# Kernel tuning notes

Measured on AMD Instinct MI355X. Metric: run time of the kernel, lower is better.

Reference implementation:

```python
import jax, jax.numpy as jnp
import numpy as np
from jax import lax

FEAT_STRIDE = 16
PRE_NMS_TOP_N = 6000   # cfg['TEST'].RPN_PRE_NMS_TOP_N
POST_NMS_TOP_N = 300   # cfg['TEST'].RPN_POST_NMS_TOP_N
NMS_THRESH = 0.7       # cfg['TEST'].RPN_NMS_THRESH
MIN_SIZE = 16.0        # cfg['TEST'].RPN_MIN_SIZE
B, A, H, W = 32, 9, 128, 128
NEG_INF = jnp.float32(-1e30)


def _whctrs(a):
    w = a[2] - a[0] + 1.0
    h = a[3] - a[1] + 1.0
    return w, h, a[0] + 0.5 * (w - 1), a[1] + 0.5 * (h - 1)

def _mkanchors(ws, hs, xc, yc):
    ws = ws[:, None]; hs = hs[:, None]
    return np.hstack((xc - 0.5 * (ws - 1), yc - 0.5 * (hs - 1),
                      xc + 0.5 * (ws - 1), yc + 0.5 * (hs - 1)))

def _ratio_enum(anchor, ratios):
    w, h, xc, yc = _whctrs(anchor)
    size = w * h
    ws = np.round(np.sqrt(size / ratios))
    hs = np.round(ws * ratios)
    return _mkanchors(ws, hs, xc, yc)

def _scale_enum(anchor, scales):
    w, h, xc, yc = _whctrs(anchor)
    return _mkanchors(w * scales, h * scales, xc, yc)

def generate_anchors(base_size=16, ratios=np.array([0.5, 1.0, 2.0]), scales=np.array([8.0, 16.0, 32.0])):
    base = np.array([1, 1, base_size, base_size], dtype=np.float64) - 1
    ra = _ratio_enum(base, ratios)
    return np.vstack([_scale_enum(ra[i], scales) for i in range(ra.shape[0])]).astype(np.float32)

_BASE_ANCHORS = generate_anchors()  # (A, 4)

def _all_anchors(h, w):
    sx = np.arange(w) * FEAT_STRIDE
    sy = np.arange(h) * FEAT_STRIDE
    sx, sy = np.meshgrid(sx, sy)  # row-major (h, w) matches permute(0,2,3,1) ordering
    shifts = np.stack([sx.ravel(), sy.ravel(), sx.ravel(), sy.ravel()], axis=1).astype(np.float32)
    return jnp.asarray((shifts[:, None, :] + _BASE_ANCHORS[None, :, :]).reshape(-1, 4))  # (h*w*A, 4)

# ---- bbox_transform_inv / clip_boxes ----

def _decode(anchors, deltas):
    ws = anchors[:, 2] - anchors[:, 0] + 1.0
    hs = anchors[:, 3] - anchors[:, 1] + 1.0
    cx = anchors[:, 0] + 0.5 * ws
    cy = anchors[:, 1] + 0.5 * hs
    dx, dy, dw, dh = deltas[:, 0], deltas[:, 1], deltas[:, 2], deltas[:, 3]
    pcx = dx * ws + cx
    pcy = dy * hs + cy
    pw = jnp.exp(dw) * ws
    ph = jnp.exp(dh) * hs
    return jnp.stack([pcx - 0.5 * pw, pcy - 0.5 * ph, pcx + 0.5 * pw, pcy + 0.5 * ph], axis=1)

def _clip(b, imh, imw):
    x1 = jnp.clip(b[:, 0], 0.0, imw - 1.0)
    y1 = jnp.clip(b[:, 1], 0.0, imh - 1.0)
    x2 = jnp.clip(b[:, 2], 0.0, imw - 1.0)
    y2 = jnp.clip(b[:, 3], 0.0, imh - 1.0)
    return jnp.stack([x1, y1, x2, y2], axis=1)

# ---- greedy NMS: pick top-score box, suppress IoU > thresh, repeat POST times ----

def _nms_select(boxes, scores):
    # boxes: (PRE, 4) score-sorted; scores: (PRE,)
    areas = (boxes[:, 2] - boxes[:, 0] + 1.0) * (boxes[:, 3] - boxes[:, 1] + 1.0)

    def body(i, st):
        s, keep, valid = st
        j = jnp.argmax(s)
        keep = keep.at[i].set(j)
        valid = valid.at[i].set(s[j] > NEG_INF)
        b = boxes[j]
        xx1 = jnp.maximum(b[0], boxes[:, 0])
        yy1 = jnp.maximum(b[1], boxes[:, 1])
        xx2 = jnp.minimum(b[2], boxes[:, 2])
        yy2 = jnp.minimum(b[3], boxes[:, 3])
        inter = jnp.maximum(xx2 - xx1 + 1.0, 0.0) * jnp.maximum(yy2 - yy1 + 1.0, 0.0)
        iou = inter / jnp.maximum(areas[j] + areas - inter, 1e-6)
        s = jnp.where(iou > NMS_THRESH, NEG_INF, s)  # suppresses j itself (IoU = 1)
        return s, keep, valid

    init = (scores, jnp.zeros((POST_NMS_TOP_N,), jnp.int32), jnp.zeros((POST_NMS_TOP_N,), bool))
    _, keep, valid = lax.fori_loop(0, POST_NMS_TOP_N, body, init)
    return keep, valid

def _per_image(sc, dl, info, anchors):
    prop = _clip(_decode(anchors, dl), info[0], info[1])  # (K*A, 4)
    ws = prop[:, 2] - prop[:, 0] + 1.0
    hs = prop[:, 3] - prop[:, 1] + 1.0
    min_sz = MIN_SIZE * info[2]
    sc = jnp.where((ws >= min_sz) & (hs >= min_sz), sc, NEG_INF)
    top_s, top_i = lax.top_k(sc, PRE_NMS_TOP_N)
    cand = prop[top_i]  # (PRE, 4)
    keep, valid = _nms_select(cand, top_s)
    return cand[keep] * valid[:, None].astype(cand.dtype)  # zero-pad invalid rows

def _forward(rpn_cls_prob, rpn_bbox_pred, im_info):
    b, _, h, w = rpn_cls_prob.shape
    anchors = _all_anchors(h, w)
    scores = rpn_cls_prob[:, A:, :, :].transpose(0, 2, 3, 1).reshape(b, -1)  # (b, h*w*A)
    deltas = rpn_bbox_pred.transpose(0, 2, 3, 1).reshape(b, -1, 4)           # (b, h*w*A, 4)
    boxes = jax.vmap(lambda s, d, i: _per_image(s, d, i, anchors))(scores, deltas, im_info)
    ids = jnp.broadcast_to(jnp.arange(b, dtype=boxes.dtype)[:, None, None], (b, POST_NMS_TOP_N, 1))
    return jnp.concatenate([ids, boxes], axis=2)  # (b, POST, 5): [batch_idx, x1, y1, x2, y2]

def setup_inputs() -> dict:
    key = jax.random.key(0)
    k1, k2 = jax.random.split(key)
    rpn_cls_prob = jax.random.uniform(k1, (B, 2 * A, H, W), dtype=jnp.float32)
    rpn_bbox_pred = jax.random.normal(k2, (B, 4 * A, H, W), dtype=jnp.float32) * 0.2
    im_info = jnp.tile(jnp.array([[H * FEAT_STRIDE, W * FEAT_STRIDE, 1.0]], dtype=jnp.float32), (B, 1))
    return {"rpn_cls_prob": rpn_cls_prob, "rpn_bbox_pred": rpn_bbox_pred, "im_info": im_info}

def reference(rpn_cls_prob, rpn_bbox_pred, im_info):
    return _forward(rpn_cls_prob, rpn_bbox_pred, im_info)
```

## Files before the change

kernel.cpp:

```cpp
#include <hip/hip_runtime.h>
#include <cstdint>
#include <cstddef>

#pragma clang fp contract(off)

typedef unsigned long long u64;

#define NB 32
#define NA 9
#define NH 128
#define NW 128
#define HW (NH*NW)
#define NANCH (NA*HW)
#define PRE_N 6000
#define POST_N 300
#define CAND_CAP 8192
#define NMS_T 0.7f
#define GX_GATHER 24
#define NBOX 6144
#define CH 512

__constant__ float c_wa[9] = {184.f,368.f,736.f,128.f,256.f,512.f,88.f,176.f,352.f};
__constant__ float c_ha[9] = {96.f,192.f,384.f,128.f,256.f,512.f,176.f,352.f,704.f};

__device__ __forceinline__ float4 decode_clip(int a, int h, int w,
    float dx, float dy, float dlw, float dlh, float imh, float imw) {
  float wa = c_wa[a], ha = c_ha[a];
  float cx = (float)w * 16.0f + 8.0f;
  float cy = (float)h * 16.0f + 8.0f;
  float pcx = dx * wa + cx;
  float pcy = dy * ha + cy;
  float pw = expf(dlw) * wa;
  float ph = expf(dlh) * ha;
  float x1 = pcx - 0.5f * pw;
  float y1 = pcy - 0.5f * ph;
  float x2 = pcx + 0.5f * pw;
  float y2 = pcy + 0.5f * ph;
  float4 r;
  r.x = fminf(fmaxf(x1, 0.0f), imw - 1.0f);
  r.y = fminf(fmaxf(y1, 0.0f), imh - 1.0f);
  r.z = fminf(fmaxf(x2, 0.0f), imw - 1.0f);
  r.w = fminf(fmaxf(y2, 0.0f), imh - 1.0f);
  return r;
}

__device__ __forceinline__ unsigned score_key(float sc, float bw, float bh, float msz) {
  unsigned bits = __float_as_uint(sc);
  unsigned key = (bits & 0x80000000u) ? ~bits : (bits | 0x80000000u);
  if (!(bw >= msz && bh >= msz)) key = 0u;
  return key;
}

__device__ __forceinline__ bool sup_test4(float4 v, float ar, float4 p, float pa) {
  float xx1 = fmaxf(p.x, v.x), yy1 = fmaxf(p.y, v.y);
  float xx2 = fminf(p.z, v.z), yy2 = fminf(p.w, v.w);
  float iw = fmaxf(xx2 - xx1 + 1.0f, 0.0f);
  float ih = fmaxf(yy2 - yy1 + 1.0f, 0.0f);
  float inter = iw * ih;
  float iou = inter / fmaxf(pa + ar - inter, 1e-6f);
  return iou > NMS_T;
}

__device__ __forceinline__ u64 shfl_xor_u64(u64 x, int m) {
  int lo = __shfl_xor((int)(unsigned)x, m, 64);
  int hi = __shfl_xor((int)(unsigned)(x >> 32), m, 64);
  return ((u64)(unsigned)hi << 32) | (unsigned)lo;
}

__device__ __forceinline__ void reg_step(u64 v[8], int t, int k, int j) {
  #pragma unroll
  for (int r = 0; r < 8; ++r) {
    if ((r & j) == 0) {
      int e = (t << 3) + r;
      bool up = ((e & k) == 0);
      u64 x = v[r], y = v[r | j];
      u64 mx = x > y ? x : y, mn = x > y ? y : x;
      v[r]     = up ? mx : mn;
      v[r | j] = up ? mn : mx;
    }
  }
}

__device__ __forceinline__ void shfl_step(u64 v[8], int t, int k, int j) {
  int m = j >> 3;
  bool lower = ((t & m) == 0);
  #pragma unroll
  for (int r = 0; r < 8; ++r) {
    int e = (t << 3) + r;
    bool up = ((e & k) == 0);
    u64 pv = shfl_xor_u64(v[r], m);
    bool keepmax = (up == lower);
    u64 x = v[r];
    u64 mx = x > pv ? x : pv, mn = x > pv ? pv : x;
    v[r] = keepmax ? mx : mn;
  }
}

__device__ __forceinline__ void lds_step(u64* sm, u64 v[8], int t, int k, int j) {
  int m = j >> 3;
  __syncthreads();
  #pragma unroll
  for (int r = 0; r < 8; ++r) sm[(r << 10) | t] = v[r];
  __syncthreads();
  bool lower = ((t & m) == 0);
  bool up = (((t << 3) & k) == 0);
  bool keepmax = (up == lower);
  int pt = t ^ m;
  #pragma unroll
  for (int r = 0; r < 8; ++r) {
    u64 pv = sm[(r << 10) | pt];
    u64 x = v[r];
    u64 mx = x > pv ? x : pv, mn = x > pv ? pv : x;
    v[r] = keepmax ? mx : mn;
  }
}

__device__ void find_B(const unsigned* __restrict__ hb, unsigned* part,
                       unsigned* outB, unsigned* outCum) {
  int tid = threadIdx.x;
  unsigned s = 0;
  for (int i = 0; i < 16; ++i) s += hb[tid*16 + i];
  part[tid] = s;
  __syncthreads();
  for (int off = 1; off < 256; off <<= 1) {
    unsigned v = (tid + off < 256) ? part[tid + off] : 0u;
    __syncthreads();
    part[tid] += v;
    __syncthreads();
  }
  unsigned St = part[tid];
  unsigned Sn = (tid < 255) ? part[tid + 1] : 0u;
  if (St >= (unsigned)PRE_N && Sn < (unsigned)PRE_N) {
    unsigned cum = Sn, B = 0, cumAbove = Sn;
    for (int i = 15; i >= 0; --i) {
      unsigned v = hb[tid*16 + i];
      if (cum + v >= (unsigned)PRE_N) { B = (unsigned)(tid*16 + i); cumAbove = cum; break; }
      cum += v;
    }
    *outB = B; *outCum = cumAbove;
  }
  __syncthreads();
}

__device__ void find_thr(const unsigned* __restrict__ hb2, unsigned B, unsigned cum0,
                         unsigned* part, unsigned* outThr) {
  int tid = threadIdx.x;
  unsigned s = 0;
  for (int i = 0; i < 16; ++i) s += hb2[tid*16 + i];
  part[tid] = s;
  __syncthreads();
  for (int off = 1; off < 256; off <<= 1) {
    unsigned v = (tid + off < 256) ? part[tid + off] : 0u;
    __syncthreads();
    part[tid] += v;
    __syncthreads();
  }
  unsigned St = cum0 + part[tid];
  unsigned Sn = cum0 + ((tid < 255) ? part[tid + 1] : 0u);
  if (St >= (unsigned)PRE_N && Sn < (unsigned)PRE_N) {
    unsigned cum = Sn, t = 1u;
    for (int i = 15; i >= 0; --i) {
      unsigned v = hb2[tid*16 + i];
      if (cum + v >= (unsigned)PRE_N) {
        t = (B << 20) | ((unsigned)(tid*16 + i) << 8);
        break;
      }
      cum += v;
    }
    if (t == 0u) t = 1u;
    *outThr = t;
  }
  __syncthreads();
}

__global__ __launch_bounds__(256) void k_keys(const float* __restrict__ cls,
    const float* __restrict__ dl, const float* __restrict__ info,
    unsigned* __restrict__ keys, unsigned* __restrict__ hist) {
  __shared__ unsigned hsh[4096];
  int tid = threadIdx.x;
  for (int i = tid; i < 4096; i += 256) hsh[i] = 0;
  int t = blockIdx.x * 256 + tid;
  int b = blockIdx.y;
  int hw0 = t * 4;
  int h = hw0 >> 7;
  const float* dlb  = dl  + (size_t)b * (4*NA*HW);
  const float* clsb = cls + (size_t)b * (2*NA*HW);
  float imh = info[b*3+0], imw = info[b*3+1];
  float msz = 16.0f * info[b*3+2];
  unsigned* kb = keys + (size_t)b * NANCH;
  __syncthreads();
  #pragma unroll
  for (int a = 0; a < 9; ++a) {
    float4 dx4 = *(const float4*)&dlb[(a*4+0)*HW + hw0];
    float4 dy4 = *(const float4*)&dlb[(a*4+1)*HW + hw0];
    float4 dw4 = *(const float4*)&dlb[(a*4+2)*HW + hw0];
    float4 dh4 = *(const float4*)&dlb[(a*4+3)*HW + hw0];
    float4 sc4 = *(const float4*)&clsb[(NA+a)*HW + hw0];
    uint4 out;
    {
      float4 bx = decode_clip(a, h, (hw0+0)&127, dx4.x, dy4.x, dw4.x, dh4.x, imh, imw);
      out.x = score_key(sc4.x, bx.z-bx.x+1.0f, bx.w-bx.y+1.0f, msz);
    }
    {
      float4 bx = decode_clip(a, h, (hw0+1)&127, dx4.y, dy4.y, dw4.y, dh4.y, imh, imw);
      out.y = score_key(sc4.y, bx.z-bx.x+1.0f, bx.w-bx.y+1.0f, msz);
    }
    {
      float4 bx = decode_clip(a, h, (hw0+2)&127, dx4.z, dy4.z, dw4.z, dh4.z, imh, imw);
      out.z = score_key(sc4.z, bx.z-bx.x+1.0f, bx.w-bx.y+1.0f, msz);
    }
    {
      float4 bx = decode_clip(a, h, (hw0+3)&127, dx4.w, dy4.w, dw4.w, dh4.w, imh, imw);
      out.w = score_key(sc4.w, bx.z-bx.x+1.0f, bx.w-bx.y+1.0f, msz);
    }
    *(uint4*)&kb[a*HW + hw0] = out;
    atomicAdd(&hsh[out.x >> 20], 1u);
    atomicAdd(&hsh[out.y >> 20], 1u);
    atomicAdd(&hsh[out.z >> 20], 1u);
    atomicAdd(&hsh[out.w >> 20], 1u);
  }
  __syncthreads();
  unsigned* gb = hist + ((size_t)b << 12);
  for (int i = tid; i < 4096; i += 256) {
    unsigned v = hsh[i];
    if (v) atomicAdd(&gb[i], v);
  }
}

__global__ __launch_bounds__(256) void k_hist2(const unsigned* __restrict__ keys,
    const unsigned* __restrict__ hist1, unsigned* __restrict__ hist2) {
  __shared__ unsigned h[4096];
  __shared__ unsigned part[256];
  __shared__ unsigned sB, sCum;
  int b = blockIdx.y, tid = threadIdx.x;
  for (int i = tid; i < 4096; i += 256) h[i] = 0;
  __syncthreads();
  find_B(hist1 + ((size_t)b << 12), part, &sB, &sCum);
  unsigned B = sB;
  const unsigned* kb = keys + (size_t)b * NANCH;
  for (int i = blockIdx.x * 256 + tid; i < NANCH; i += gridDim.x * 256) {
    unsigned k = kb[i];
    if ((k >> 20) == B) atomicAdd(&h[(k >> 8) & 4095u], 1u);
  }
  __syncthreads();
  unsigned* gb = hist2 + ((size_t)b << 12);
  for (int i = tid; i < 4096; i += 256) { unsigned v = h[i]; if (v) atomicAdd(&gb[i], v); }
}

__global__ __launch_bounds__(256) void k_gather(const unsigned* __restrict__ keys,
    const unsigned* __restrict__ hist1, const unsigned* __restrict__ hist2,
    const float* __restrict__ dl, const float* __restrict__ info,
    unsigned* __restrict__ cnt, u64* __restrict__ cand,
    float4* __restrict__ boxes) {
  int b = blockIdx.y, tid = threadIdx.x;
  int lane = tid & 63, wv = tid >> 6;
  __shared__ unsigned part[256];
  __shared__ unsigned sB, sCum, sThr;
  __shared__ unsigned wcnt[4], woff[4], blkbase;
  if (tid == 0) sThr = 1u;
  __syncthreads();
  find_B(hist1 + ((size_t)b << 12), part, &sB, &sCum);
  find_thr(hist2 + ((size_t)b << 12), sB, sCum, part, &sThr);
  unsigned t_ = sThr;
  const unsigned* kb = keys + (size_t)b * NANCH;
  const float* dlb = dl + (size_t)b * (4*NA*HW);
  float imh = info[b*3+0], imw = info[b*3+1];
  u64* cb = cand + (size_t)b * CAND_CAP;
  float4* bxc = boxes + (size_t)b * CAND_CAP;
  unsigned* cp = cnt + (size_t)b * 64;
  const int PER_BLK = NANCH / GX_GATHER;
  int base0 = blockIdx.x * PER_BLK;
  for (int it = 0; it < PER_BLK / 256; ++it) {
    int j = base0 + it * 256 + tid;
    unsigned key = kb[j];
    bool pass = key >= t_;
    u64 mask = __ballot(pass);
    if (lane == 0) wcnt[wv] = (unsigned)__popcll(mask);
    __syncthreads();
    if (tid == 0) {
      unsigned s0 = 0;
      for (int w = 0; w < 4; ++w) { woff[w] = s0; s0 += wcnt[w]; }
      blkbase = s0 ? atomicAdd(cp, s0) : 0u;
    }
    __syncthreads();
    if (pass) {
      unsigned pos = blkbase + woff[wv] + (unsigned)__popcll(mask & ((1ull << lane) - 1ull));
      if (pos < CAND_CAP) {
        int a = j >> 14, hw = j & (HW - 1);
        unsigned oi = (unsigned)(hw * 9 + a);
        unsigned noi = (~oi) & 0x3FFFFu;
        cb[pos] = ((u64)key << 32) | ((u64)noi << 13) | (u64)pos;
        bxc[pos] = decode_clip(a, hw >> 7, hw & 127,
                               dlb[(a*4+0)*HW + hw], dlb[(a*4+1)*HW + hw],
                               dlb[(a*4+2)*HW + hw], dlb[(a*4+3)*HW + hw],
                               imh, imw);
      }
    }
    __syncthreads();
  }
}

__global__ __launch_bounds__(1024) void k_final6(const u64* __restrict__ cand,
    const unsigned* __restrict__ cnt, const float4* __restrict__ boxes,
    float* __restrict__ out) {
  __shared__ float4 bx[NBOX];
  __shared__ float4 cbox2[CH];
  __shared__ float  carea2[CH];
  __shared__ float4 kbox[POST_N];
  __shared__ float  karea[POST_N];
  __shared__ u64 sup[CH][9];
  __shared__ u64 aliveM[8];
  __shared__ u64 kgW[8];
  __shared__ int s_nk;
  u64* sm = (u64*)bx;

  int b = blockIdx.x, tid = threadIdx.x;
  int lane = tid & 63, wv = tid >> 6;
  if (tid == 0) s_nk = 0;

  unsigned effcnt = cnt[b * 64];
  if (effcnt > CAND_CAP) effcnt = CAND_CAP;
  const u64* cb = cand + (size_t)b * CAND_CAP;
  int e0 = tid << 3;
  u64 v[8];
  #pragma unroll
  for (int r = 0; r < 8; ++r)
    v[r] = ((unsigned)(e0 + r) < effcnt) ? cb[e0 + r] : 0ull;

  for (int k = 2; k <= 8; k <<= 1)
    for (int j = k >> 1; j >= 1; j >>= 1) reg_step(v, tid, k, j);
  for (int k = 16; k <= CAND_CAP; k <<= 1) {
    int j = k >> 1;
    for (; j >= 512; j >>= 1) lds_step(sm, v, tid, k, j);
    for (; j >= 8;   j >>= 1) shfl_step(v, tid, k, j);
    for (; j >= 1;   j >>= 1) reg_step(v, tid, k, j);
  }
  __syncthreads();

  const float4* bxc = boxes + (size_t)b * CAND_CAP;
  #pragma unroll
  for (int r = 0; r < 8; ++r) {
    int rank = e0 + r;
    if (rank < NBOX) {
      u64 ck = (rank < PRE_N) ? v[r] : 0ull;
      float4 w = make_float4(0.f, 0.f, -1.f, -1.f);
      if ((unsigned)(ck >> 32) != 0u)
        w = bxc[(unsigned)(ck & 0x1FFFu)];
      bx[rank] = w;
    }
  }
  __syncthreads();

  float4 mybx[6];
  float  myar[6];
  int deadm = 0;
  #pragma unroll
  for (int m = 0; m < 6; ++m) {
    float4 w = bx[tid + (m << 10)];
    mybx[m] = w;
    float wid = w.z - w.x + 1.0f;
    myar[m] = wid * (w.w - w.y + 1.0f);
    if (!(wid > 0.0f)) deadm |= (1 << m);
  }

  float* ob = out + (size_t)b * (POST_N * 5);
  int c512 = tid & (CH - 1);
  int seg = tid >> 9;
  bool done = false;

  #pragma unroll
  for (int m = 0; m < 6; ++m) {
    #pragma unroll
    for (int par = 0; par < 2; ++par) {
      if (done) continue;
      int nk0 = s_nk;

      bool own = (tid >> 9) == par;
      int cc = tid - (par << 9);
      bool alive = own && !((deadm >> m) & 1);
      {
        u64 am = __ballot(alive);
        if (own && lane == 0) aliveM[wv & 7] = am;
      }
      __syncthreads();

      int na = 0;
      #pragma unroll
      for (int g = 0; g < 8; ++g) na += (int)__popcll(aliveM[g]);
      if (na == 0) continue;

      if (alive) {
        int cg2 = cc >> 6;
        int pre = 0;
        #pragma unroll
        for (int g = 0; g < 8; ++g) if (g < cg2) pre += (int)__popcll(aliveM[g]);
        pre += (int)__popcll(aliveM[cg2] & ((1ull << (cc & 63)) - 1ull));
        cbox2[pre] = mybx[m];
        carea2[pre] = myar[m];
      }
      __syncthreads();

      {
        int i = c512;
        if (i < na) {
          int ngi = (i >> 6) + 1;
          int gA = seg ? (ngi >> 1) : 0;
          int gB = seg ? ngi : (ngi >> 1);
          if (gA < gB) {
            float4 vi = cbox2[i];
            float ai = carea2[i];
            for (int g = gA; g < gB; ++g) {
              int jmax = i - (g << 6);
              if (jmax > 64) jmax = 64;
              u64 r = 0;
              #pragma unroll 4
              for (int j = 0; j < jmax; ++j) {
                if (sup_test4(vi, ai, cbox2[(g << 6) + j], carea2[(g << 6) + j]))
                  r |= 1ull << j;
              }
              sup[i][g] = r;
            }
          }
        }
      }
      __syncthreads();

      if (tid < 64) {
        u64 kw[8];
        int nst = (na + 63) >> 6;
        u64 srow[8];
        {
          const u64* rp = sup[lane];
          #pragma unroll
          for (int g = 0; g < 8; ++g) srow[g] = rp[g];
        }
        #pragma unroll
        for (int s = 0; s < 8; ++s) {
          u64 nsr[8];
          bool pf = (s + 1 < nst);
          if (pf) {
            const u64* rp = sup[(s + 1) * 64 + lane];
            #pragma unroll
            for (int g = 0; g < 8; ++g) nsr[g] = rp[g];
          }
          u64 kg = 0;
          if (s < nst) {
            int cc2 = s * 64 + lane;
            bool a = (cc2 < na);
            u64 blocked = 0;
            #pragma unroll
            for (int g = 0; g < 8; ++g) if (g < s) blocked |= (srow[g] & kw[g]);
            a = a && (blocked == 0ull);
            u64 r = a ? srow[s] : 0ull;
            u64 cm = __ballot(a);
            while (cm) {
              int j = __builtin_ctzll(cm);
              kg |= 1ull << j;
              u64 rem = __ballot((r >> j) & 1ull);
              cm &= ~(rem | (1ull << j));
            }
          }
          kw[s] = kg;
          if (pf) {
            #pragma unroll
            for (int g = 0; g < 8; ++g) srow[g] = nsr[g];
          }
        }
        if (lane == 0) {
          #pragma unroll
          for (int s = 0; s < 8; ++s) kgW[s] = kw[s];
        }
      }
      __syncthreads();

      if (tid < na) {
        int s = tid >> 6;
        u64 kgw = kgW[s];
        bool kept = (kgw >> (tid & 63)) & 1;
        int pre = 0;
        #pragma unroll
        for (int g = 0; g < 8; ++g) if (g < s) pre += (int)__popcll(kgW[g]);
        pre += (int)__popcll(kgw & ((1ull << (tid & 63)) - 1ull));
        int rank = nk0 + pre;
        if (kept && rank < POST_N) {
          float4 ww = cbox2[tid];
          kbox[rank] = ww; karea[rank] = carea2[tid];
          ob[rank*5+0] = (float)b;
          ob[rank*5+1] = ww.x; ob[rank*5+2] = ww.y; ob[rank*5+3] = ww.z; ob[rank*5+4] = ww.w;
        }
      }
      if (tid == 0) {
        int tot = 0;
        #pragma unroll
        for (int s = 0; s < 8; ++s) tot += (int)__popcll(kgW[s]);
        int nn = nk0 + tot;
        s_nk = nn < POST_N ? nn : POST_N;
      }
      __syncthreads();

      int nk1 = s_nk;
      if (nk1 >= POST_N) { done = true; continue; }
      if (nk1 > nk0) {
        #pragma unroll
        for (int m2 = m; m2 < 6; ++m2) {
          bool fut = (m2 > m) || ((tid >> 9) > par);
          if (fut && !((deadm >> m2) & 1)) {
            for (int k = nk0; k < nk1; ++k) {
              if (sup_test4(mybx[m2], myar[m2], kbox[k], karea[k])) {
                deadm |= (1 << m2);
                break;
              }
            }
          }
        }
      }
    }
  }
  __syncthreads();
  int nk = s_nk;
  for (int r = nk + tid; r < POST_N; r += 1024) {
    ob[r*5+0] = (float)b;
    ob[r*5+1] = 0.f; ob[r*5+2] = 0.f; ob[r*5+3] = 0.f; ob[r*5+4] = 0.f;
  }
}

extern "C" void kernel_launch(void* const* d_in, const int* in_sizes, int n_in,
                              void* d_out, int out_size, void* d_ws, size_t ws_size,
                              hipStream_t stream) {
  const float* cls  = (const float*)d_in[0];
  const float* dl   = (const float*)d_in[1];
  const float* info = (const float*)d_in[2];
  float* out = (float*)d_out;
  char* ws = (char*)d_ws;

  const size_t OFF_KEYS = 0;
  const size_t OFF_H1   = 18874368;
  const size_t OFF_H2   = 19398656;
  const size_t OFF_CNT  = 19922944;
  const size_t OFF_CAND = 19931136;
  const size_t OFF_BOX  = 22028288;
  const size_t WS_NEED  = 26222592;
  if (ws_size < WS_NEED) return;

  unsigned* keys  = (unsigned*)(ws + OFF_KEYS);
  unsigned* h1    = (unsigned*)(ws + OFF_H1);
  unsigned* h2    = (unsigned*)(ws + OFF_H2);
  unsigned* cnt   = (unsigned*)(ws + OFF_CNT);
  u64* cand = (u64*)(ws + OFF_CAND);
  float4* boxes = (float4*)(ws + OFF_BOX);

  hipMemsetAsync(ws + OFF_H1, 0, OFF_CAND - OFF_H1, stream);

  dim3 g1(HW / 1024, NB);
  k_keys<<<g1, 256, 0, stream>>>(cls, dl, info, keys, h1);
  dim3 gh(8, NB);
  k_hist2<<<gh, 256, 0, stream>>>(keys, h1, h2);
  dim3 gg(GX_GATHER, NB);
  k_gather<<<gg, 256, 0, stream>>>(keys, h1, h2, dl, info, cnt, cand, boxes);
  k_final6<<<NB, 1024, 0, stream>>>(cand, cnt, boxes, out);
}
```

Measured before the change: 337.5 us.

## Split bitonic sort into parallel presort kernel plus final merge stages

Result: faster. 315.3 us (-6.6%).

```diff
diff --git a/kernel.cpp b/kernel.cpp
--- a/kernel.cpp
+++ b/kernel.cpp
@@ -109,6 +109,54 @@
   #pragma unroll
   for (int r = 0; r < 8; ++r) {
     u64 pv = sm[(r << 10) | pt];
+    u64 x = v[r];
+    u64 mx = x > pv ? x : pv, mn = x > pv ? pv : x;
+    v[r] = keepmax ? mx : mn;
+  }
+}
+
+__device__ __forceinline__ void p_reg(u64 v[4], int t, int k, int j, bool flip) {
+  #pragma unroll
+  for (int r = 0; r < 4; ++r) {
+    if ((r & j) == 0) {
+      int e = (t << 2) + r;
+      bool up = (((e & k) == 0) != flip);
+      u64 x = v[r], y = v[r | j];
+      u64 mx = x > y ? x : y, mn = x > y ? y : x;
+      v[r]     = up ? mx : mn;
+      v[r | j] = up ? mn : mx;
+    }
+  }
+}
+
+__device__ __forceinline__ void p_shfl(u64 v[4], int t, int k, int j, bool flip) {
+  int m = j >> 2;
+  bool lower = ((t & m) == 0);
+  #pragma unroll
+  for (int r = 0; r < 4; ++r) {
+    int e = (t << 2) + r;
+    bool up = (((e & k) == 0) != flip);
+    u64 pv = shfl_xor_u64(v[r], m);
+    bool keepmax = (up == lower);
+    u64 x = v[r];
+    u64 mx = x > pv ? x : pv, mn = x > pv ? pv : x;
+    v[r] = keepmax ? mx : mn;
+  }
+}
+
+__device__ __forceinline__ void p_lds(u64* sm, u64 v[4], int t, int k, int j, bool flip) {
+  int m = j >> 2;
+  __syncthreads();
+  #pragma unroll
+  for (int r = 0; r < 4; ++r) sm[(r << 9) | t] = v[r];
+  __syncthreads();
+  bool lower = ((t & m) == 0);
+  bool up = ((((t << 2) & k) == 0) != flip);
+  bool keepmax = (up == lower);
+  int pt = t ^ m;
+  #pragma unroll
+  for (int r = 0; r < 4; ++r) {
+    u64 pv = sm[(r << 9) | pt];
     u64 x = v[r];
     u64 mx = x > pv ? x : pv, mn = x > pv ? pv : x;
     v[r] = keepmax ? mx : mn;
@@ -300,9 +348,34 @@
   }
 }
 
-__global__ __launch_bounds__(1024) void k_final6(const u64* __restrict__ cand,
-    const unsigned* __restrict__ cnt, const float4* __restrict__ boxes,
-    float* __restrict__ out) {
+__global__ __launch_bounds__(512) void k_presort(u64* __restrict__ cand,
+                                                 const unsigned* __restrict__ cnt) {
+  __shared__ u64 sm[2048];
+  int blk = blockIdx.x;
+  int b = blk >> 2, q = blk & 3;
+  bool flip = (q & 1) != 0;
+  unsigned effcnt = cnt[b * 64];
+  if (effcnt > CAND_CAP) effcnt = CAND_CAP;
+  u64* cb = cand + (size_t)b * CAND_CAP + (size_t)q * 2048;
+  int base = q * 2048;
+  int t = threadIdx.x;
+  int e0 = t << 2;
+  u64 v[4];
+  #pragma unroll
+  for (int r = 0; r < 4; ++r)
+    v[r] = ((unsigned)(base + e0 + r) < effcnt) ? cb[e0 + r] : 0ull;
+  for (int k = 2; k <= 2048; k <<= 1) {
+    int j = k >> 1;
+    for (; j >= 256; j >>= 1) p_lds(sm, v, t, k, j, flip);
+    for (; j >= 4;   j >>= 1) p_shfl(v, t, k, j, flip);
+    for (; j >= 1;   j >>= 1) p_reg(v, t, k, j, flip);
+  }
+  #pragma unroll
+  for (int r = 0; r < 4; ++r) cb[e0 + r] = v[r];
+}
+
+__global__ __launch_bounds__(1024) void k_final7(const u64* __restrict__ cand,
+    const float4* __restrict__ boxes, float* __restrict__ out) {
   __shared__ float4 bx[NBOX];
   __shared__ float4 cbox2[CH];
   __shared__ float  carea2[CH];
@@ -318,18 +391,13 @@
   int lane = tid & 63, wv = tid >> 6;
   if (tid == 0) s_nk = 0;
 
-  unsigned effcnt = cnt[b * 64];
-  if (effcnt > CAND_CAP) effcnt = CAND_CAP;
   const u64* cb = cand + (size_t)b * CAND_CAP;
   int e0 = tid << 3;
   u64 v[8];
   #pragma unroll
-  for (int r = 0; r < 8; ++r)
-    v[r] = ((unsigned)(e0 + r) < effcnt) ? cb[e0 + r] : 0ull;
-
-  for (int k = 2; k <= 8; k <<= 1)
-    for (int j = k >> 1; j >= 1; j >>= 1) reg_step(v, tid, k, j);
-  for (int k = 16; k <= CAND_CAP; k <<= 1) {
+  for (int r = 0; r < 8; ++r) v[r] = cb[e0 + r];
+
+  for (int k = 4096; k <= CAND_CAP; k <<= 1) {
     int j = k >> 1;
     for (; j >= 512; j >>= 1) lds_step(sm, v, tid, k, j);
     for (; j >= 8;   j >>= 1) shfl_step(v, tid, k, j);
@@ -557,5 +625,6 @@
   k_hist2<<<gh, 256, 0, stream>>>(keys, h1, h2);
   dim3 gg(GX_GATHER, NB);
   k_gather<<<gg, 256, 0, stream>>>(keys, h1, h2, dl, info, cnt, cand, boxes);
-  k_final6<<<NB, 1024, 0, stream>>>(cand, cnt, boxes, out);
-}
+  k_presort<<<NB * 4, 512, 0, stream>>>(cand, cnt);
+  k_final7<<<NB, 1024, 0, stream>>>(cand, boxes, out);
+}
```
